# Optimization experiments

Hardware: AMD Instinct MI355X
Metric: run time of the kernel (lower is better)

Reference implementation:

```python
import jax, jax.numpy as jnp
import numpy as np

N = 64
L = 4096
STEP = 0.001


def _make_dplr_hippo(n):
    # Standard S4 DPLR HiPPO-LegS construction (numpy, done once at setup).
    q = np.arange(n, dtype=np.float64)
    col = np.sqrt(1.0 + 2.0 * q)
    A = -(np.tril(col[:, None] * col[None, :]) - np.diag(q))
    P = np.sqrt(q + 0.5)
    B = np.sqrt(2.0 * q + 1.0)
    S = A + P[:, None] * P[None, :]
    lam_re = np.mean(np.diag(S)) * np.ones(n)
    lam_im, V = np.linalg.eigh(S * -1j)
    Pc = V.conj().T @ P
    Bc = V.conj().T @ B
    return lam_re, lam_im, Pc, Bc


def setup_inputs() -> dict:
    key = jax.random.key(0)
    k1, k2 = jax.random.split(key)
    x = jax.random.normal(k1, (16, 256, L), dtype=jnp.float32)
    lam_re, lam_im, Pc, Bc = _make_dplr_hippo(N)
    Cp = np.asarray(jax.random.normal(k2, (N, 2), dtype=jnp.float32)) * 0.5 ** 0.5
    return {
        "x": x,
        "Lambda_re": jnp.asarray(lam_re, dtype=jnp.float32),
        "Lambda_im": jnp.asarray(lam_im, dtype=jnp.float32),
        "P_re": jnp.asarray(Pc.real, dtype=jnp.float32),
        "P_im": jnp.asarray(Pc.imag, dtype=jnp.float32),
        "B_re": jnp.asarray(Bc.real, dtype=jnp.float32),
        "B_im": jnp.asarray(Bc.imag, dtype=jnp.float32),
        "C_re": jnp.asarray(Cp[:, 0], dtype=jnp.float32),
        "C_im": jnp.asarray(Cp[:, 1], dtype=jnp.float32),
    }


def _fourier_kernel(Lambda, P, B, C, step, length):
    # Frequency-domain DPLR SSM kernel (Annotated-S4 kernel_DPLR, at the roots of unity).
    Omega = jnp.exp(-2j * jnp.pi * jnp.arange(length) / length).astype(jnp.complex64)  # [L]
    g = (2.0 / step) * ((1.0 - Omega) / (1.0 + Omega))  # bilinear-transform frequencies [L]
    c = 2.0 / (1.0 + Omega)
    denom = 1.0 / (g[:, None] - Lambda[None, :])  # Cauchy matrix [L, N]
    k00 = denom @ (jnp.conj(C) * B)
    k01 = denom @ (jnp.conj(C) * P)
    k10 = denom @ (jnp.conj(P) * B)  # Q = P in this module
    k11 = denom @ (jnp.conj(P) * P)
    return c * (k00 - k01 * (1.0 / (1.0 + k11)) * k10)  # [L] complex64


def reference(x, Lambda_re, Lambda_im, P_re, P_im, B_re, B_im, C_re, C_im):
    Lambda = (Lambda_re + 1j * Lambda_im).astype(jnp.complex64)
    P = (P_re + 1j * P_im).astype(jnp.complex64)
    B = (B_re + 1j * B_im).astype(jnp.complex64)
    C = (C_re + 1j * C_im).astype(jnp.complex64)
    K = _fourier_kernel(Lambda, P, B, C, STEP, L)  # [L]
    fft_u = jnp.fft.fft(x, n=L)                    # [batch, ch, L] complex64
    y = jnp.fft.ifft(K * fft_u, n=L)
    return y.real.astype(x.dtype)
```

## Files before the change

kernel.cpp:

```cpp
#include <hip/hip_runtime.h>
#include <math.h>

#define LEN 4096
#define NSTATE 64

__device__ inline float2 cmulf(float2 a, float2 b){
  return make_float2(a.x*b.x - a.y*b.y, a.x*b.y + a.y*b.x);
}

__global__ void s4_kernelA1(const float* __restrict__ Lre, const float* __restrict__ Lim,
                            const float* __restrict__ Pre, const float* __restrict__ Pim,
                            const float* __restrict__ Bre, const float* __restrict__ Bim,
                            const float* __restrict__ Cre, const float* __restrict__ Cim,
                            float2* __restrict__ Kout) {
  int k = blockIdx.x * blockDim.x + threadIdx.x;
  if (k >= LEN) return;
  double ang = -2.0 * M_PI * (double)k / (double)LEN;
  double orr = cos(ang), oi = sin(ang);
  double dr = 1.0 + orr, di = oi;
  double d2 = dr*dr + di*di;
  double nr = 1.0 - orr, ni = -oi;
  double gr = 2000.0 * (nr*dr + ni*di) / d2;
  double gi = 2000.0 * (ni*dr - nr*di) / d2;
  double cr = 2.0 * dr / d2, ci = -2.0 * di / d2;
  double k00r=0,k00i=0,k01r=0,k01i=0,k10r=0,k10i=0,k11r=0,k11i=0;
  for (int n = 0; n < NSTATE; ++n) {
    double lr = Lre[n], li = Lim[n];
    double pr = Pre[n], pi = Pim[n];
    double br = Bre[n], bi = Bim[n];
    double qr = Cre[n], qi = Cim[n];
    double er = gr - lr, ei = gi - li;
    double e2 = er*er + ei*ei;
    double den_r = er / e2, den_i = -ei / e2;
    double cbr = qr*br + qi*bi, cbi = qr*bi - qi*br;
    double cpr = qr*pr + qi*pi, cpi = qr*pi - qi*pr;
    double pbr = pr*br + pi*bi, pbi = pr*bi - pi*br;
    double ppr = pr*pr + pi*pi;
    k00r += den_r*cbr - den_i*cbi; k00i += den_r*cbi + den_i*cbr;
    k01r += den_r*cpr - den_i*cpi; k01i += den_r*cpi + den_i*cpr;
    k10r += den_r*pbr - den_i*pbi; k10i += den_r*pbi + den_i*pbr;
    k11r += den_r*ppr;             k11i += den_i*ppr;
  }
  double ar = 1.0 + k11r, ai = k11i;
  double a2 = ar*ar + ai*ai;
  double ivr = ar/a2, ivi = -ai/a2;
  double mr = k01r*k10r - k01i*k10i, mi = k01r*k10i + k01i*k10r;
  double tr = mr*ivr - mi*ivi, ti = mr*ivi + mi*ivr;
  double sr = k00r - tr, si = k00i - ti;
  double Kr = cr*sr - ci*si, Ki = cr*si + ci*sr;
  Kout[k] = make_float2((float)Kr, (float)Ki);
}

__global__ void s4_kernelA2(const float2* __restrict__ Kin, float2* __restrict__ keff_br) {
  int p = blockIdx.x * blockDim.x + threadIdx.x;
  if (p >= LEN) return;
  int k = 0, pp = p;
  #pragma unroll
  for (int i = 0; i < 6; ++i) { k = (k << 2) | (pp & 3); pp >>= 2; }
  int kneg = (LEN - k) & (LEN - 1);
  float2 a = Kin[k], b = Kin[kneg];
  const float s = 0.5f / (float)LEN;
  keff_br[p] = make_float2(s * (a.x + b.x), s * (a.y - b.y));
}

__launch_bounds__(256)
__global__ void s4_fftconv(const float* __restrict__ x, const float2* __restrict__ keff_br,
                           float* __restrict__ out) {
  __shared__ float2 X[LEN];
  const int t = threadIdx.x;
  const size_t base = (size_t)blockIdx.x * 2 * LEN;
  const float* x1 = x + base;
  const float* x2 = x1 + LEN;

  #pragma unroll
  for (int i = 0; i < 16; ++i) {
    int idx = t + 256*i;
    X[idx] = make_float2(x1[idx], x2[idx]);
  }
  __syncthreads();

  for (int n = LEN; n >= 4; n >>= 2) {
    const int q = n >> 2;
    const float fac = -6.28318530717958647692f / (float)n;
    #pragma unroll
    for (int it = 0; it < 4; ++it) {
      int m = t + 256*it;
      int j = m & (q - 1);
      int i0 = 4*m - 3*j;
      float2 a0 = X[i0], a1 = X[i0+q], a2 = X[i0+2*q], a3 = X[i0+3*q];
      float2 t0 = make_float2(a0.x+a2.x, a0.y+a2.y);
      float2 t1 = make_float2(a0.x-a2.x, a0.y-a2.y);
      float2 t2 = make_float2(a1.x+a3.x, a1.y+a3.y);
      float2 t3 = make_float2(a1.x-a3.x, a1.y-a3.y);
      float2 y0 = make_float2(t0.x+t2.x, t0.y+t2.y);
      float2 y1 = make_float2(t1.x+t3.y, t1.y-t3.x);
      float2 y2 = make_float2(t0.x-t2.x, t0.y-t2.y);
      float2 y3 = make_float2(t1.x-t3.y, t1.y+t3.x);
      float ang = fac * (float)j;
      float s1, c1;
      __sincosf(ang, &s1, &c1);
      float2 w1 = make_float2(c1, s1);
      float2 w2 = cmulf(w1, w1);
      float2 w3 = cmulf(w2, w1);
      X[i0]     = y0;
      X[i0+q]   = cmulf(y1, w1);
      X[i0+2*q] = cmulf(y2, w2);
      X[i0+3*q] = cmulf(y3, w3);
    }
    __syncthreads();
  }

  #pragma unroll
  for (int it = 0; it < 4; ++it) {
    int m = t + 256*it;
    int i0 = 4*m;
    float2 u0 = cmulf(X[i0],   keff_br[i0]);
    float2 u1 = cmulf(X[i0+1], keff_br[i0+1]);
    float2 u2 = cmulf(X[i0+2], keff_br[i0+2]);
    float2 u3 = cmulf(X[i0+3], keff_br[i0+3]);
    float2 t0 = make_float2(u0.x+u2.x, u0.y+u2.y);
    float2 t1 = make_float2(u0.x-u2.x, u0.y-u2.y);
    float2 t2 = make_float2(u1.x+u3.x, u1.y+u3.y);
    float2 t3 = make_float2(u1.x-u3.x, u1.y-u3.y);
    X[i0]   = make_float2(t0.x+t2.x, t0.y+t2.y);
    X[i0+1] = make_float2(t1.x-t3.y, t1.y+t3.x);
    X[i0+2] = make_float2(t0.x-t2.x, t0.y-t2.y);
    X[i0+3] = make_float2(t1.x+t3.y, t1.y-t3.x);
  }
  __syncthreads();

  for (int n = 16; n <= LEN; n <<= 2) {
    const int q = n >> 2;
    const float fac = 6.28318530717958647692f / (float)n;
    #pragma unroll
    for (int it = 0; it < 4; ++it) {
      int m = t + 256*it;
      int j = m & (q - 1);
      int i0 = 4*m - 3*j;
      float ang = fac * (float)j;
      float s1, c1;
      __sincosf(ang, &s1, &c1);
      float2 w1 = make_float2(c1, s1);
      float2 w2 = cmulf(w1, w1);
      float2 w3 = cmulf(w2, w1);
      float2 u0 = X[i0];
      float2 u1 = cmulf(X[i0+q],   w1);
      float2 u2 = cmulf(X[i0+2*q], w2);
      float2 u3 = cmulf(X[i0+3*q], w3);
      float2 t0 = make_float2(u0.x+u2.x, u0.y+u2.y);
      float2 t1 = make_float2(u0.x-u2.x, u0.y-u2.y);
      float2 t2 = make_float2(u1.x+u3.x, u1.y+u3.y);
      float2 t3 = make_float2(u1.x-u3.x, u1.y-u3.y);
      X[i0]     = make_float2(t0.x+t2.x, t0.y+t2.y);
      X[i0+q]   = make_float2(t1.x-t3.y, t1.y+t3.x);
      X[i0+2*q] = make_float2(t0.x-t2.x, t0.y-t2.y);
      X[i0+3*q] = make_float2(t1.x+t3.y, t1.y-t3.x);
    }
    __syncthreads();
  }

  float* o1 = out + base;
  float* o2 = o1 + LEN;
  #pragma unroll
  for (int i = 0; i < 16; ++i) {
    int idx = t + 256*i;
    float2 v = X[idx];
    o1[idx] = v.x;
    o2[idx] = v.y;
  }
}

extern "C" void kernel_launch(void* const* d_in, const int* in_sizes, int n_in,
                              void* d_out, int out_size, void* d_ws, size_t ws_size,
                              hipStream_t stream) {
  const float* x   = (const float*)d_in[0];
  const float* Lre = (const float*)d_in[1];
  const float* Lim = (const float*)d_in[2];
  const float* Pre = (const float*)d_in[3];
  const float* Pim = (const float*)d_in[4];
  const float* Bre = (const float*)d_in[5];
  const float* Bim = (const float*)d_in[6];
  const float* Cre = (const float*)d_in[7];
  const float* Cim = (const float*)d_in[8];
  float* out = (float*)d_out;

  float2* Kws     = (float2*)d_ws;
  float2* keff_br = Kws + LEN;

  s4_kernelA1<<<LEN/256, 256, 0, stream>>>(Lre, Lim, Pre, Pim, Bre, Bim, Cre, Cim, Kws);
  s4_kernelA2<<<LEN/256, 256, 0, stream>>>(Kws, keff_br);

  const int rows = out_size / LEN;
  s4_fftconv<<<rows/2, 256, 0, stream>>>(x, keff_br, out);
}
```

Before: 181.9 us.

## Parallelize Cauchy kernel over state dimension with wavefront shuffle reduction

```diff
diff --git a/kernel.cpp b/kernel.cpp
--- a/kernel.cpp
+++ b/kernel.cpp
@@ -8,47 +8,60 @@
   return make_float2(a.x*b.x - a.y*b.y, a.x*b.y + a.y*b.x);
 }
 
-__global__ void s4_kernelA1(const float* __restrict__ Lre, const float* __restrict__ Lim,
-                            const float* __restrict__ Pre, const float* __restrict__ Pim,
-                            const float* __restrict__ Bre, const float* __restrict__ Bim,
-                            const float* __restrict__ Cre, const float* __restrict__ Cim,
-                            float2* __restrict__ Kout) {
-  int k = blockIdx.x * blockDim.x + threadIdx.x;
-  if (k >= LEN) return;
+__global__ __launch_bounds__(64)
+void s4_kernelA1(const float* __restrict__ Lre, const float* __restrict__ Lim,
+                 const float* __restrict__ Pre, const float* __restrict__ Pim,
+                 const float* __restrict__ Bre, const float* __restrict__ Bim,
+                 const float* __restrict__ Cre, const float* __restrict__ Cim,
+                 float2* __restrict__ Kout) {
+  const int k = blockIdx.x;
+  const int n = threadIdx.x;
+
   double ang = -2.0 * M_PI * (double)k / (double)LEN;
   double orr = cos(ang), oi = sin(ang);
   double dr = 1.0 + orr, di = oi;
   double d2 = dr*dr + di*di;
   double nr = 1.0 - orr, ni = -oi;
-  double gr = 2000.0 * (nr*dr + ni*di) / d2;
-  double gi = 2000.0 * (ni*dr - nr*di) / d2;
-  double cr = 2.0 * dr / d2, ci = -2.0 * di / d2;
-  double k00r=0,k00i=0,k01r=0,k01i=0,k10r=0,k10i=0,k11r=0,k11i=0;
-  for (int n = 0; n < NSTATE; ++n) {
-    double lr = Lre[n], li = Lim[n];
-    double pr = Pre[n], pi = Pim[n];
-    double br = Bre[n], bi = Bim[n];
-    double qr = Cre[n], qi = Cim[n];
-    double er = gr - lr, ei = gi - li;
-    double e2 = er*er + ei*ei;
-    double den_r = er / e2, den_i = -ei / e2;
-    double cbr = qr*br + qi*bi, cbi = qr*bi - qi*br;
-    double cpr = qr*pr + qi*pi, cpi = qr*pi - qi*pr;
-    double pbr = pr*br + pi*bi, pbi = pr*bi - pi*br;
-    double ppr = pr*pr + pi*pi;
-    k00r += den_r*cbr - den_i*cbi; k00i += den_r*cbi + den_i*cbr;
-    k01r += den_r*cpr - den_i*cpi; k01i += den_r*cpi + den_i*cpr;
-    k10r += den_r*pbr - den_i*pbi; k10i += den_r*pbi + den_i*pbr;
-    k11r += den_r*ppr;             k11i += den_i*ppr;
-  }
-  double ar = 1.0 + k11r, ai = k11i;
-  double a2 = ar*ar + ai*ai;
-  double ivr = ar/a2, ivi = -ai/a2;
-  double mr = k01r*k10r - k01i*k10i, mi = k01r*k10i + k01i*k10r;
-  double tr = mr*ivr - mi*ivi, ti = mr*ivi + mi*ivr;
-  double sr = k00r - tr, si = k00i - ti;
-  double Kr = cr*sr - ci*si, Ki = cr*si + ci*sr;
-  Kout[k] = make_float2((float)Kr, (float)Ki);
+  double inv_d2 = 1.0 / d2;
+  double gr = 2000.0 * (nr*dr + ni*di) * inv_d2;
+  double gi = 2000.0 * (ni*dr - nr*di) * inv_d2;
+  double cr = 2.0 * dr * inv_d2, ci = -2.0 * di * inv_d2;
+
+  double lr = Lre[n], li = Lim[n];
+  double pr = Pre[n], pi = Pim[n];
+  double br = Bre[n], bi = Bim[n];
+  double qr = Cre[n], qi = Cim[n];
+  double er = gr - lr, ei = gi - li;
+  double inv_e2 = 1.0 / (er*er + ei*ei);
+  double den_r = er * inv_e2, den_i = -ei * inv_e2;
+  double cbr = qr*br + qi*bi, cbi = qr*bi - qi*br;
+  double cpr = qr*pr + qi*pi, cpi = qr*pi - qi*pr;
+  double pbr = pr*br + pi*bi, pbi = pr*bi - pi*br;
+  double ppr = pr*pr + pi*pi;
+
+  double k00r = den_r*cbr - den_i*cbi, k00i = den_r*cbi + den_i*cbr;
+  double k01r = den_r*cpr - den_i*cpi, k01i = den_r*cpi + den_i*cpr;
+  double k10r = den_r*pbr - den_i*pbi, k10i = den_r*pbi + den_i*pbr;
+  double k11r = den_r*ppr,             k11i = den_i*ppr;
+
+  #pragma unroll
+  for (int off = 32; off >= 1; off >>= 1) {
+    k00r += __shfl_xor(k00r, off); k00i += __shfl_xor(k00i, off);
+    k01r += __shfl_xor(k01r, off); k01i += __shfl_xor(k01i, off);
+    k10r += __shfl_xor(k10r, off); k10i += __shfl_xor(k10i, off);
+    k11r += __shfl_xor(k11r, off); k11i += __shfl_xor(k11i, off);
+  }
+
+  if (n == 0) {
+    double ar = 1.0 + k11r, ai = k11i;
+    double inv_a2 = 1.0 / (ar*ar + ai*ai);
+    double ivr = ar*inv_a2, ivi = -ai*inv_a2;
+    double mr = k01r*k10r - k01i*k10i, mi = k01r*k10i + k01i*k10r;
+    double tr = mr*ivr - mi*ivi, ti = mr*ivi + mi*ivr;
+    double sr = k00r - tr, si = k00i - ti;
+    double Kr = cr*sr - ci*si, Ki = cr*si + ci*sr;
+    Kout[k] = make_float2((float)Kr, (float)Ki);
+  }
 }
 
 __global__ void s4_kernelA2(const float2* __restrict__ Kin, float2* __restrict__ keff_br) {
@@ -187,7 +200,7 @@
   float2* Kws     = (float2*)d_ws;
   float2* keff_br = Kws + LEN;
 
-  s4_kernelA1<<<LEN/256, 256, 0, stream>>>(Lre, Lim, Pre, Pim, Bre, Bim, Cre, Cim, Kws);
+  s4_kernelA1<<<LEN, 64, 0, stream>>>(Lre, Lim, Pre, Pim, Bre, Bim, Cre, Cim, Kws);
   s4_kernelA2<<<LEN/256, 256, 0, stream>>>(Kws, keff_br);
 
   const int rows = out_size / LEN;
```

Measured after the change: 160.6 us. -11.7%, faster.
